# Kernel tuning notes

Hardware: AMD Instinct MI355X
Metric: run time of the kernel (lower is better)

Reference implementation:

```python
import jax, jax.numpy as jnp
import numpy as np

IFZ = 256      # in_features
SFZ = 1280     # sequence_features
AHZ = 8        # attention heads
AFZ = 64       # attention feature dim per head
NRES = 20      # canonical_num_residues
SCALE = float(np.sqrt(AFZ))
RESID = float(np.sqrt(2.0))
EPS = 1e-6


def _ln(x, s, b, eps=1e-5):
    m = jnp.mean(x, axis=-1, keepdims=True)
    v = jnp.var(x, axis=-1, keepdims=True)
    return (x - m) / jnp.sqrt(v + eps) * s + b


def setup_inputs() -> dict:
    key = jax.random.key(0)
    ks = jax.random.split(key, 20)
    N, B, S = 4096, 4, 512
    HD = AHZ * AFZ
    w = lambda k, shp: (jax.random.normal(k, shp, jnp.float32) * 0.02)
    d = {}
    d["x"] = jax.random.normal(ks[0], (N, IFZ), jnp.float32)
    d["packed_sequence_emb"] = jax.random.normal(ks[1], (B, S, SFZ), jnp.float32)
    d["packed_sequence_mask"] = jnp.ones((B, S), jnp.float32)
    d["prot_mask"] = jnp.arange(N, dtype=jnp.int32)
    d["batch"] = jax.random.randint(ks[2], (N,), 0, B, jnp.int32)
    # projections (bias=False)
    d["Wq"] = w(ks[3], (HD, IFZ))
    d["Wk"] = w(ks[4], (HD, SFZ))
    d["Wv"] = w(ks[5], (HD, SFZ))
    # ag: LayerNorm(HD) -> Linear(HD, IFZ, bias=False) (dropout = identity at eval)
    d["ag_ln_s"] = jnp.ones((HD,), jnp.float32)
    d["ag_ln_b"] = jnp.zeros((HD,), jnp.float32)
    d["Wag"] = w(ks[6], (IFZ, HD))
    d["res_ln_s"] = jnp.ones((3, IFZ), jnp.float32)
    d["res_ln_b"] = jnp.zeros((3, IFZ), jnp.float32)
    d["res_w1"] = w(ks[7], (3, IFZ, IFZ))
    d["res_b1"] = jnp.zeros((3, IFZ), jnp.float32)
    d["res_w2"] = w(ks[8], (3, IFZ, IFZ))
    d["res_b2"] = jnp.zeros((3, IFZ), jnp.float32)
    d["head_w"] = w(ks[9], (NRES, IFZ))
    d["head_b"] = jnp.zeros((NRES,), jnp.float32)
    # output LayerNorm en
    d["en_s"] = jnp.ones((IFZ,), jnp.float32)
    d["en_b"] = jnp.zeros((IFZ,), jnp.float32)
    return d


def _forward(x, emb, mask, prot_mask, batch, Wq, Wk, Wv, ag_ln_s, ag_ln_b, Wag,
             res_ln_s, res_ln_b, res_w1, res_b1, res_w2, res_b2,
             head_w, head_b, en_s, en_b):
    N = x.shape[0]
    B, S = emb.shape[:2]
    b_idx = batch[prot_mask]                      # [M]
    xp = x[prot_mask]                             # [M, IFZ]
    M = xp.shape[0]
    q = (xp @ Wq.T).reshape(M, AHZ, AFZ)          # [M,H,D]
    k = (emb @ Wk.T).reshape(B, S, AHZ, AFZ)      # [B,S,H,D]
    v = (emb @ Wv.T).reshape(B, S, AHZ, AFZ)
    # score vs every protein, then pick own protein (avoids materializing [M,S,H,D] gather)
    scores_all = jnp.einsum('mhd,bshd->mbsh', q, k) / SCALE          # [M,B,S,H]
    sel = b_idx[:, None, None, None]
    scores = jnp.take_along_axis(scores_all, sel, axis=1)[:, 0]       # [M,S,H]
    mb = mask[b_idx][:, :, None]                                      # [M,S,1]
    # padded_sequence_softmax: softmax over S, zero pads, renormalize
    sm = jax.nn.softmax(scores, axis=1) * mb
    w = sm / (jnp.sum(sm, axis=1, keepdims=True) + EPS)               # [M,S,H]
    feat_all = jnp.einsum('msh,bshd->mbhd', w, v)                     # [M,B,H,D]
    feat = jnp.take_along_axis(feat_all, sel, axis=1)[:, 0]
    feat = feat.reshape(M, AHZ * AFZ)
    ag = _ln(feat, ag_ln_s, ag_ln_b) @ Wag.T                          # [M, IFZ]
    # seq_aa_head on the scattered new features (identical to ag for unique prot_mask)
    h = ag
    for i in range(3):
        y = _ln(h, res_ln_s[i], res_ln_b[i])
        y = jax.nn.relu(y @ res_w1[i].T + res_b1[i])
        y = y @ res_w2[i].T + res_b2[i]
        h = (h + y) / RESID
    logits = h @ head_w.T + head_b                                     # [M, NRES]
    new_features = jnp.zeros_like(x).at[prot_mask].set(ag)
    seq_aa_logits = jnp.zeros((N, NRES), x.dtype).at[prot_mask].set(logits)
    unpacked_scores = jnp.zeros((N, S, AHZ), x.dtype).at[prot_mask].set(scores)
    out_x = _ln(x + new_features / RESID, en_s, en_b)
    return out_x, seq_aa_logits, unpacked_scores


def reference(x, packed_sequence_emb, packed_sequence_mask, prot_mask, batch,
              Wq, Wk, Wv, ag_ln_s, ag_ln_b, Wag,
              res_ln_s, res_ln_b, res_w1, res_b1, res_w2, res_b2,
              head_w, head_b, en_s, en_b):
    return _forward(x, packed_sequence_emb, packed_sequence_mask, prot_mask, batch,
                    Wq, Wk, Wv, ag_ln_s, ag_ln_b, Wag,
                    res_ln_s, res_ln_b, res_w1, res_b1, res_w2, res_b2,
                    head_w, head_b, en_s, en_b)
```

## Files before the change

kernel.cpp:

```cpp
#include <hip/hip_runtime.h>
#include <math.h>


typedef short bf8 __attribute__((ext_vector_type(8)));
typedef short bf4 __attribute__((ext_vector_type(4)));
typedef float f32x4 __attribute__((ext_vector_type(4)));
typedef unsigned short u16;

constexpr int LDT = 40;
enum { EPI_NONE = 0, EPI_BIAS_RELU = 1, EPI_BIAS = 2, EPI_RESID = 3 };
#define RSQRT2 0.70710678118654752f

__device__ __forceinline__ u16 f2bf(float f) {
  unsigned int u = __builtin_bit_cast(unsigned int, f);
  unsigned int r = u + 0x7fffu + ((u >> 16) & 1u);
  return (u16)(r >> 16);
}
__device__ __forceinline__ float bf2f(u16 v) {
  return __builtin_bit_cast(float, (unsigned int)v << 16);
}
__device__ __forceinline__ f32x4 mfma16(bf8 a, bf8 b, f32x4 c) {
  return __builtin_amdgcn_mfma_f32_16x16x32_bf16(a, b, c, 0, 0, 0);
}

struct CvtDesc { const float* src; u16* dst; int n; };
struct CvtArgs { CvtDesc d[8]; };

__global__ __launch_bounds__(256) void cvt_k(CvtArgs a) {
  CvtDesc d = a.d[blockIdx.z];
  int i = (blockIdx.x * 256 + threadIdx.x) * 8;
  if (i >= d.n) return;
  f32x4 v0 = *(const f32x4*)(d.src + i);
  f32x4 v1 = *(const f32x4*)(d.src + i + 4);
  bf8 o;
  o[0] = (short)f2bf(v0[0]); o[1] = (short)f2bf(v0[1]);
  o[2] = (short)f2bf(v0[2]); o[3] = (short)f2bf(v0[3]);
  o[4] = (short)f2bf(v1[0]); o[5] = (short)f2bf(v1[1]);
  o[6] = (short)f2bf(v1[2]); o[7] = (short)f2bf(v1[3]);
  *(bf8*)(d.dst + i) = o;
}

template <int EPI, bool BFOUT>
__global__ __launch_bounds__(256) void mgemm2(
    const u16* __restrict__ A, const u16* __restrict__ B,
    void* __restrict__ Cv, int M, int N, int K, int lda, int ldb, int ldc,
    const float* __restrict__ bias, const float* __restrict__ Hin,
    const int* __restrict__ gatherA, const int* __restrict__ scatterC) {
  __shared__ __align__(16) u16 As[128 * LDT];
  __shared__ __align__(16) u16 Bs[64 * LDT];
  const int tid = threadIdx.x;
  const int m0 = blockIdx.y * 128, n0 = blockIdx.x * 64;
  const int wave = tid >> 6, lane = tid & 63;
  const int wm = (wave & 1) * 64, wn = (wave >> 1) * 32;
  const int lrow = lane & 15, quad = lane >> 4;
  const int srow = tid >> 2, skq = tid & 3;

  int gr0 = m0 + srow, gr1 = m0 + srow + 64;
  int ar0 = (gr0 < M) ? (gatherA ? gatherA[gr0] : gr0) : -1;
  int ar1 = (gr1 < M) ? (gatherA ? gatherA[gr1] : gr1) : -1;
  const u16* Ap0 = (ar0 >= 0) ? A + (size_t)ar0 * lda + skq * 8 : nullptr;
  const u16* Ap1 = (ar1 >= 0) ? A + (size_t)ar1 * lda + skq * 8 : nullptr;
  const u16* Bp = (n0 + srow < N) ? B + (size_t)(n0 + srow) * ldb + skq * 8 : nullptr;
  u16* AsW0 = &As[srow * LDT + skq * 8];
  u16* AsW1 = &As[(srow + 64) * LDT + skq * 8];
  u16* BsW = &Bs[srow * LDT + skq * 8];

  f32x4 acc[4][2];
#pragma unroll
  for (int i = 0; i < 4; ++i)
#pragma unroll
    for (int j = 0; j < 2; ++j) acc[i][j] = (f32x4){0.f, 0.f, 0.f, 0.f};
  const bf8 z8 = {0, 0, 0, 0, 0, 0, 0, 0};

  for (int k0 = 0; k0 < K; k0 += 32) {
    bf8 a0 = Ap0 ? *(const bf8*)(Ap0 + k0) : z8;
    bf8 a1 = Ap1 ? *(const bf8*)(Ap1 + k0) : z8;
    bf8 bv = Bp ? *(const bf8*)(Bp + k0) : z8;
    *(bf8*)AsW0 = a0;
    *(bf8*)AsW1 = a1;
    *(bf8*)BsW = bv;
    __syncthreads();
    bf8 af[4], bfr[2];
#pragma unroll
    for (int i = 0; i < 4; ++i)
      af[i] = *(const bf8*)&As[(wm + i * 16 + lrow) * LDT + quad * 8];
#pragma unroll
    for (int j = 0; j < 2; ++j)
      bfr[j] = *(const bf8*)&Bs[(wn + j * 16 + lrow) * LDT + quad * 8];
#pragma unroll
    for (int i = 0; i < 4; ++i)
#pragma unroll
      for (int j = 0; j < 2; ++j) acc[i][j] = mfma16(af[i], bfr[j], acc[i][j]);
    __syncthreads();
  }

  float* Cf = (float*)Cv;
  u16* Cb = (u16*)Cv;
#pragma unroll
  for (int i = 0; i < 4; ++i) {
#pragma unroll
    for (int r = 0; r < 4; ++r) {
      int row = m0 + wm + i * 16 + quad * 4 + r;
      if (row >= M) continue;
      if (gatherA && gatherA[row] < 0) continue;
      int orow = scatterC ? scatterC[row] : row;
#pragma unroll
      for (int j = 0; j < 2; ++j) {
        int col = n0 + wn + j * 16 + lrow;
        if (col >= N) continue;
        float v = acc[i][j][r];
        if (EPI == EPI_BIAS_RELU) v = fmaxf(v + bias[col], 0.f);
        else if (EPI == EPI_BIAS) v += bias[col];
        else if (EPI == EPI_RESID) v = (Hin[(size_t)row * ldc + col] + v + bias[col]) * RSQRT2;
        if (BFOUT) Cb[(size_t)orow * ldc + col] = f2bf(v);
        else Cf[(size_t)orow * ldc + col] = v;
      }
    }
  }
}

__global__ __launch_bounds__(256) void vtrans(const u16* __restrict__ KV,
                                              u16* __restrict__ VT) {
  __shared__ u16 t[32][33];
  int b = blockIdx.z;
  int s0 = blockIdx.x * 32, d0 = blockIdx.y * 32;
  int tx = threadIdx.x & 31, ty = threadIdx.x >> 5;
#pragma unroll
  for (int i = 0; i < 32; i += 8)
    t[ty + i][tx] = KV[(size_t)(b * 512 + s0 + ty + i) * 1024 + 512 + d0 + tx];
  __syncthreads();
#pragma unroll
  for (int i = 0; i < 32; i += 8)
    VT[(size_t)(b * 512 + d0 + ty + i) * 512 + s0 + tx] = t[tx][ty + i];
}

constexpr int WST = 520;
constexpr int QST = 72;

__global__ __launch_bounds__(256) void attn_fused(
    const u16* __restrict__ Q, const u16* __restrict__ KV,
    const u16* __restrict__ VT, const int* __restrict__ list,
    const float* __restrict__ mask, u16* __restrict__ packed,
    u16* __restrict__ feat, int N) {
  const int b = blockIdx.y >> 3, h = blockIdx.y & 7;
  const int mt = blockIdx.x;
  const int* lst = list + (size_t)b * N + mt * 32;
  if (lst[0] < 0) return;

  __shared__ __align__(16) u16 Ws[32 * WST];
  __shared__ __align__(16) u16 Qs[32 * QST];
  __shared__ __align__(16) u16 KVs[64 * QST];
  __shared__ __align__(16) float mk[8][68];
  __shared__ int mS[32];

  const int tid = threadIdx.x;
  const int wave = tid >> 6, lane = tid & 63;
  const int wm = (wave & 1) * 16, wns = (wave >> 1) * 32;
  const int lrow = lane & 15, quad = lane >> 4;
  const bf8 z8 = {0, 0, 0, 0, 0, 0, 0, 0};

  const int c0 = tid * 2, c1 = tid * 2 + 1;
  const int sr0 = c0 >> 3, kq0 = c0 & 7;
  const int sr1 = c1 >> 3, kq1 = c1 & 7;
  u16* kvw0 = &KVs[sr0 * QST + kq0 * 8];
  u16* kvw1 = &KVs[sr1 * QST + kq1 * 8];

  if (tid < 32) mS[tid] = lst[tid];
  {
    int p = tid >> 5, j = (tid & 31) * 2;
    *(float2*)&mk[p][j] = *(const float2*)&mask[(size_t)b * 512 + p * 64 + j];
  }
  {
    int qr = tid >> 3, kq = tid & 7;
    int m = lst[qr];
    *(bf8*)&Qs[qr * QST + kq * 8] =
        (m >= 0) ? *(const bf8*)(Q + (size_t)m * 512 + h * 64 + kq * 8) : z8;
  }
  const u16* KVb = KV + (size_t)(b * 512) * 1024 + h * 64;
  {
    int sta = mt & 7;
    *(bf8*)kvw0 = *(const bf8*)(KVb + (size_t)(sta * 64 + sr0) * 1024 + kq0 * 8);
    *(bf8*)kvw1 = *(const bf8*)(KVb + (size_t)(sta * 64 + sr1) * 1024 + kq1 * 8);
  }
  __syncthreads();

  const bf8 qa0 = *(const bf8*)&Qs[(wm + lrow) * QST + 0 + quad * 8];
  const bf8 qa1 = *(const bf8*)&Qs[(wm + lrow) * QST + 32 + quad * 8];

  bf8 r0, r1;
  for (int st = 0; st < 8; ++st) {
    const int sta = (st + mt) & 7;
    if (st < 7) {
      int nx = (st + 1 + mt) & 7;
      r0 = *(const bf8*)(KVb + (size_t)(nx * 64 + sr0) * 1024 + kq0 * 8);
      r1 = *(const bf8*)(KVb + (size_t)(nx * 64 + sr1) * 1024 + kq1 * 8);
    }
    f32x4 acc0 = {0.f, 0.f, 0.f, 0.f}, acc1 = acc0;
    {
      bf8 b00 = *(const bf8*)&KVs[(wns + lrow) * QST + quad * 8];
      bf8 b10 = *(const bf8*)&KVs[(wns + 16 + lrow) * QST + quad * 8];
      bf8 b01 = *(const bf8*)&KVs[(wns + lrow) * QST + 32 + quad * 8];
      bf8 b11 = *(const bf8*)&KVs[(wns + 16 + lrow) * QST + 32 + quad * 8];
      __builtin_amdgcn_s_setprio(1);
      acc0 = mfma16(qa0, b00, acc0);
      acc1 = mfma16(qa0, b10, acc1);
      acc0 = mfma16(qa1, b01, acc0);
      acc1 = mfma16(qa1, b11, acc1);
      __builtin_amdgcn_s_setprio(0);
    }
#pragma unroll
    for (int r = 0; r < 4; ++r) {
      int lr = wm + quad * 4 + r;
      Ws[lr * WST + sta * 64 + wns + lrow] = f2bf(acc0[r] * 0.125f);
      Ws[lr * WST + sta * 64 + wns + 16 + lrow] = f2bf(acc1[r] * 0.125f);
    }
    __syncthreads();
    if (st < 7) {
      *(bf8*)kvw0 = r0;
      *(bf8*)kvw1 = r1;
      __syncthreads();
    }
  }

  const u16* VTb = VT + (size_t)(b * 512 + h * 64) * 512;
  bf8 v0p = *(const bf8*)(VTb + (size_t)sr0 * 512 + ((mt & 7) << 6) + kq0 * 8);
  bf8 v1p = *(const bf8*)(VTb + (size_t)sr1 * 512 + ((mt & 7) << 6) + kq1 * 8);

  {
    const int row = tid >> 3, part = tid & 7;
    u16* wrow = &Ws[row * WST + part * 64];
    const int mm = mS[row];
    bf8 w[8];
    float mx = -1e30f;
#pragma unroll
    for (int v = 0; v < 8; ++v) {
      w[v] = *(const bf8*)(wrow + v * 8);
#pragma unroll
      for (int j = 0; j < 8; ++j) mx = fmaxf(mx, bf2f((u16)w[v][j]));
    }
    if (mm >= 0) {
      u16* prow = packed + ((size_t)h * N + mm) * 512 + part * 64;
#pragma unroll
      for (int v = 0; v < 8; ++v) *(bf8*)(prow + v * 8) = w[v];
    }
#pragma unroll
    for (int d = 1; d < 8; d <<= 1) mx = fmaxf(mx, __shfl_xor(mx, d));
    float ev[64];
    float se = 0.f, ms = 0.f;
#pragma unroll
    for (int v = 0; v < 8; ++v) {
      f32x4 m0 = *(const f32x4*)&mk[part][v * 8];
      f32x4 m1 = *(const f32x4*)&mk[part][v * 8 + 4];
#pragma unroll
      for (int j = 0; j < 8; ++j) {
        float e = __expf(bf2f((u16)w[v][j]) - mx);
        ev[v * 8 + j] = e;
        se += e;
        ms += e * (j < 4 ? m0[j] : m1[j - 4]);
      }
    }
#pragma unroll
    for (int d = 1; d < 8; d <<= 1) {
      se += __shfl_xor(se, d);
      ms += __shfl_xor(ms, d);
    }
    float iv = 1.0f / (ms + 1e-6f * se);
#pragma unroll
    for (int v = 0; v < 8; ++v) {
      f32x4 m0 = *(const f32x4*)&mk[part][v * 8];
      f32x4 m1 = *(const f32x4*)&mk[part][v * 8 + 4];
      bf8 o;
#pragma unroll
      for (int j = 0; j < 8; ++j)
        o[j] = (short)f2bf(ev[v * 8 + j] * (j < 4 ? m0[j] : m1[j - 4]) * iv);
      *(bf8*)(wrow + v * 8) = o;
    }
  }
  __syncthreads();
  *(bf8*)kvw0 = v0p;
  *(bf8*)kvw1 = v1p;
  __syncthreads();

  f32x4 acc0 = {0.f, 0.f, 0.f, 0.f}, acc1 = acc0;
  for (int ss = 0; ss < 8; ++ss) {
    const int s0 = ((ss + mt) & 7) << 6;
    if (ss < 7) {
      int nx = ((ss + 1 + mt) & 7) << 6;
      v0p = *(const bf8*)(VTb + (size_t)sr0 * 512 + nx + kq0 * 8);
      v1p = *(const bf8*)(VTb + (size_t)sr1 * 512 + nx + kq1 * 8);
    }
#pragma unroll
    for (int k0 = 0; k0 < 64; k0 += 32) {
      bf8 a = *(const bf8*)&Ws[(wm + lrow) * WST + s0 + k0 + quad * 8];
      bf8 b0 = *(const bf8*)&KVs[(wns + lrow) * QST + k0 + quad * 8];
      bf8 b1 = *(const bf8*)&KVs[(wns + 16 + lrow) * QST + k0 + quad * 8];
      __builtin_amdgcn_s_setprio(1);
      acc0 = mfma16(a, b0, acc0);
      acc1 = mfma16(a, b1, acc1);
      __builtin_amdgcn_s_setprio(0);
    }
    __syncthreads();
    if (ss < 7) {
      *(bf8*)kvw0 = v0p;
      *(bf8*)kvw1 = v1p;
      __syncthreads();
    }
  }
#pragma unroll
  for (int r = 0; r < 4; ++r) {
    int lr = wm + quad * 4 + r;
    int mm = mS[lr];
    if (mm < 0) continue;
    u16* frow = feat + (size_t)mm * 512 + h * 64;
    frow[wns + lrow] = f2bf(acc0[r]);
    frow[wns + 16 + lrow] = f2bf(acc1[r]);
  }
}

__global__ __launch_bounds__(256) void unpack_k(const u16* __restrict__ packed,
                                                const int* __restrict__ pm,
                                                float* __restrict__ out_sc,
                                                int N) {
  __shared__ u16 Ls[8 * 520];
  int m = blockIdx.x, tid = threadIdx.x;
  int h = tid >> 5, c = (tid & 31) * 16;
  const u16* row = packed + ((size_t)h * N + m) * 512 + c;
  *(bf8*)&Ls[h * 520 + c] = *(const bf8*)row;
  *(bf8*)&Ls[h * 520 + c + 8] = *(const bf8*)(row + 8);
  __syncthreads();
  float* orow = out_sc + (size_t)pm[m] * 4096;
#pragma unroll
  for (int i = 0; i < 16; ++i) {
    int e = tid + i * 256;
    orow[e] = bf2f(Ls[(e & 7) * 520 + (e >> 3)]);
  }
}

constexpr int HST = 268;
constexpr int AST = 520;
constexpr int YST = 280;

__global__ __launch_bounds__(1024) void mlp_fused(
    const u16* __restrict__ feat, const float* __restrict__ ag_s,
    const float* __restrict__ ag_b, const u16* __restrict__ Wag,
    float* __restrict__ AGout, const float* __restrict__ rls,
    const float* __restrict__ rlb, const u16* __restrict__ rw1,
    const float* __restrict__ rb1, const u16* __restrict__ rw2,
    const float* __restrict__ rb2, const float* __restrict__ hw,
    const float* __restrict__ hb, const int* __restrict__ pm,
    float* __restrict__ out_lg) {
  __shared__ __align__(16) float Hs[16 * HST];
  __shared__ __align__(16) u16 As[16 * AST];
  __shared__ __align__(16) u16 Ys[16 * YST];
  const int tid = threadIdx.x;
  const int m0 = blockIdx.x * 16;
  const int wave = tid >> 6, lane = tid & 63;
  const int lrow = lane & 15, quad = lane >> 4;
  const int wn = wave * 16;
  const int row = wave;
  const int wq8 = quad * 8;

  const u16* WagW = Wag + (size_t)(wn + lrow) * 512 + wq8;
  const u16* W1W = rw1 + (size_t)(wn + lrow) * 256 + wq8;
  const u16* W2W = rw2 + (size_t)(wn + lrow) * 256 + wq8;

  bf8 wp[8];
#pragma unroll
  for (int i = 0; i < 8; ++i) wp[i] = *(const bf8*)(WagW + i * 32);

  {
    const u16* frow = feat + (size_t)(m0 + row) * 512 + lane * 8;
    bf8 f0 = *(const bf8*)frow;
    float s = 0.f, sq = 0.f;
#pragma unroll
    for (int j = 0; j < 8; ++j) {
      float a = bf2f((u16)f0[j]);
      s += a;
      sq += a * a;
    }
#pragma unroll
    for (int d = 1; d < 64; d <<= 1) { s += __shfl_xor(s, d); sq += __shfl_xor(sq, d); }
    float mean = s * (1.0f / 512.0f);
    float var = sq * (1.0f / 512.0f) - mean * mean;
    float is = 1.0f / sqrtf(var + 1e-5f);
    int c = lane * 8;
    bf8 o0;
#pragma unroll
    for (int j = 0; j < 8; ++j)
      o0[j] = (short)f2bf((bf2f((u16)f0[j]) - mean) * is * ag_s[c + j] + ag_b[c + j]);
    *(bf8*)&As[row * AST + c] = o0;
  }
  __syncthreads();

  {
    f32x4 acc = {0.f, 0.f, 0.f, 0.f};
#pragma unroll
    for (int i = 0; i < 8; ++i) {
      bf8 a = *(const bf8*)&As[lrow * AST + i * 32 + wq8];
      acc = mfma16(a, wp[i], acc);
      wp[i] = *(const bf8*)(WagW + 256 + i * 32);
    }
#pragma unroll
    for (int i = 0; i < 8; ++i) {
      bf8 a = *(const bf8*)&As[lrow * AST + 256 + i * 32 + wq8];
      acc = mfma16(a, wp[i], acc);
      wp[i] = *(const bf8*)(W1W + i * 32);
    }
#pragma unroll
    for (int r = 0; r < 4; ++r) {
      int rr = quad * 4 + r;
      Hs[rr * HST + wn + lrow] = acc[r];
      AGout[(size_t)(m0 + rr) * 256 + wn + lrow] = acc[r];
    }
  }

  for (int layer = 0; layer < 3; ++layer) {
    __syncthreads();
    {
      int c = lane * 4;
      f32x4 h0 = *(const f32x4*)&Hs[row * HST + c];
      float s = h0[0] + h0[1] + h0[2] + h0[3];
      float sq = h0[0] * h0[0] + h0[1] * h0[1] + h0[2] * h0[2] + h0[3] * h0[3];
#pragma unroll
      for (int d = 1; d < 64; d <<= 1) { s += __shfl_xor(s, d); sq += __shfl_xor(sq, d); }
      float mean = s * (1.0f / 256.0f);
      float var = sq * (1.0f / 256.0f) - mean * mean;
      float is = 1.0f / sqrtf(var + 1e-5f);
      const float* g = rls + layer * 256;
      const float* bb = rlb + layer * 256;
      bf4 o;
#pragma unroll
      for (int e = 0; e < 4; ++e)
        o[e] = (short)f2bf((h0[e] - mean) * is * g[c + e] + bb[c + e]);
      *(bf4*)&As[row * AST + c] = o;
    }
    __syncthreads();

    {
      f32x4 acc = {0.f, 0.f, 0.f, 0.f};
#pragma unroll
      for (int i = 0; i < 8; ++i) {
        bf8 a = *(const bf8*)&As[lrow * AST + i * 32 + wq8];
        acc = mfma16(a, wp[i], acc);
        wp[i] = *(const bf8*)(W2W + (size_t)layer * 65536 + i * 32);
      }
      float bi = rb1[layer * 256 + wn + lrow];
#pragma unroll
      for (int r = 0; r < 4; ++r) {
        int rr = quad * 4 + r;
        Ys[rr * YST + wn + lrow] = f2bf(fmaxf(acc[r] + bi, 0.f));
      }
    }
    __syncthreads();

    {
      f32x4 acc = {0.f, 0.f, 0.f, 0.f};
#pragma unroll
      for (int i = 0; i < 8; ++i) {
        bf8 a = *(const bf8*)&Ys[lrow * YST + i * 32 + wq8];
        acc = mfma16(a, wp[i], acc);
        if (layer < 2)
          wp[i] = *(const bf8*)(W1W + (size_t)(layer + 1) * 65536 + i * 32);
      }
      float bi = rb2[layer * 256 + wn + lrow];
#pragma unroll
      for (int r = 0; r < 4; ++r) {
        int rr = quad * 4 + r;
        float* h0 = &Hs[rr * HST + wn + lrow];
        *h0 = (*h0 + acc[r] + bi) * RSQRT2;
      }
    }
  }
  __syncthreads();

  if (lane < 20) {
    const float* hrow = &Hs[row * HST];
    const float* wrow = hw + (size_t)lane * 256;
    float l0 = 0.f, l1 = 0.f, l2 = 0.f, l3 = 0.f;
    for (int k = 0; k < 256; k += 16) {
      f32x4 h0 = *(const f32x4*)&hrow[k];
      f32x4 h1 = *(const f32x4*)&hrow[k + 4];
      f32x4 h2 = *(const f32x4*)&hrow[k + 8];
      f32x4 h3 = *(const f32x4*)&hrow[k + 12];
      f32x4 w0 = *(const f32x4*)&wrow[k];
      f32x4 w1 = *(const f32x4*)&wrow[k + 4];
      f32x4 w2 = *(const f32x4*)&wrow[k + 8];
      f32x4 w3 = *(const f32x4*)&wrow[k + 12];
#pragma unroll
      for (int e = 0; e < 4; ++e) {
        l0 += h0[e] * w0[e];
        l1 += h1[e] * w1[e];
        l2 += h2[e] * w2[e];
        l3 += h3[e] * w3[e];
      }
    }
    out_lg[(size_t)pm[m0 + row] * 20 + lane] = l0 + l1 + l2 + l3 + hb[lane];
  }
}

__global__ __launch_bounds__(256) void outx_k(
    const float* __restrict__ x, const float* __restrict__ ag,
    const int* __restrict__ inv, const float* __restrict__ g,
    const float* __restrict__ bb, float* __restrict__ out) {
  __shared__ float red[256];
  int n = blockIdx.x, tid = threadIdx.x;
  int mi = inv[n];
  float v = x[(size_t)n * 256 + tid];
  if (mi >= 0) v += ag[(size_t)mi * 256 + tid] * RSQRT2;
  red[tid] = v;
  __syncthreads();
  for (int off = 128; off; off >>= 1) {
    if (tid < off) red[tid] += red[tid + off];
    __syncthreads();
  }
  float mean = red[0] * (1.0f / 256.0f);
  __syncthreads();
  red[tid] = v * v;
  __syncthreads();
  for (int off = 128; off; off >>= 1) {
    if (tid < off) red[tid] += red[tid + off];
    __syncthreads();
  }
  float var = red[0] * (1.0f / 256.0f) - mean * mean;
  float is = 1.0f / sqrtf(var + 1e-5f);
  out[(size_t)n * 256 + tid] = (v - mean) * is * g[tid] + bb[tid];
}

__global__ void init_idx_k(int* __restrict__ list, int* __restrict__ inv,
                           int* __restrict__ cnt, int N, int B) {
  int i = blockIdx.x * 256 + threadIdx.x;
  if (i < B * N) list[i] = -1;
  if (i < N) inv[i] = -1;
  if (i < B) cnt[i] = 0;
}

__global__ void compact_k(const int* __restrict__ pm,
                          const int* __restrict__ batch, int* __restrict__ list,
                          int* __restrict__ inv, int* __restrict__ cnt, int N) {
  int m = blockIdx.x * 256 + threadIdx.x;
  if (m >= N) return;
  int p = pm[m];
  int b = batch[p];
  int slot = atomicAdd(&cnt[b], 1);
  list[(size_t)b * N + slot] = m;
  inv[p] = m;
}

extern "C" void kernel_launch(void* const* d_in, const int* in_sizes, int n_in,
                              void* d_out, int out_size, void* d_ws,
                              size_t ws_size, hipStream_t stream) {
  const float* x = (const float*)d_in[0];
  const float* emb = (const float*)d_in[1];
  const float* mask = (const float*)d_in[2];
  const int* pm = (const int*)d_in[3];
  const int* batch = (const int*)d_in[4];
  const float* Wq = (const float*)d_in[5];
  const float* Wk = (const float*)d_in[6];
  const float* Wv = (const float*)d_in[7];
  const float* ag_s = (const float*)d_in[8];
  const float* ag_b = (const float*)d_in[9];
  const float* Wag = (const float*)d_in[10];
  const float* rls = (const float*)d_in[11];
  const float* rlb = (const float*)d_in[12];
  const float* rw1 = (const float*)d_in[13];
  const float* rb1 = (const float*)d_in[14];
  const float* rw2 = (const float*)d_in[15];
  const float* rb2 = (const float*)d_in[16];
  const float* hw = (const float*)d_in[17];
  const float* hb = (const float*)d_in[18];
  const float* ens = (const float*)d_in[19];
  const float* enb = (const float*)d_in[20];

  const int N = in_sizes[0] / 256;
  const int B = in_sizes[2] / 512;

  char* wsb = (char*)d_ws;
  u16* embbf = (u16*)(wsb + 0);
  u16* xbf   = (u16*)(wsb + 5242880);
  u16* Wkvbf = (u16*)(wsb + 7340032);
  u16* Wqbf  = (u16*)(wsb + 9961472);
  u16* packed = (u16*)(wsb + 0);
  u16* KVbf   = (u16*)(wsb + 33554432);
  u16* Qbf    = (u16*)(wsb + 37748736);
  u16* VT     = (u16*)(wsb + 41943040);
  u16* featE  = (u16*)(wsb + 44040192);
  float* AG = (float*)(wsb + 37748736);
  u16* Wagbf = (u16*)(wsb + 48234496);
  u16* rw1bf = (u16*)(wsb + 48496640);
  u16* rw2bf = (u16*)(wsb + 48889856);
  int* list  = (int*)(wsb + 49545216);
  int* inv   = (int*)(wsb + 49610752);
  int* cnt   = (int*)(wsb + 49627136);

  float* out_x = (float*)d_out;
  float* out_lg = out_x + (size_t)N * 256;
  float* out_sc = out_lg + (size_t)N * 20;

  CvtArgs ca;
  ca.d[0] = {emb, embbf, 2 * 512 * 1280 * 2};
  ca.d[1] = {x, xbf, 4096 * 256};
  ca.d[2] = {Wk, Wkvbf, 512 * 1280};
  ca.d[3] = {Wv, Wkvbf + 512 * 1280, 512 * 1280};
  ca.d[4] = {Wq, Wqbf, 512 * 256};
  ca.d[5] = {Wag, Wagbf, 256 * 512};
  ca.d[6] = {rw1, rw1bf, 3 * 256 * 256};
  ca.d[7] = {rw2, rw2bf, 3 * 256 * 256};
  cvt_k<<<dim3(1281, 1, 8), 256, 0, stream>>>(ca);
  init_idx_k<<<(B * N + 255) / 256, 256, 0, stream>>>(list, inv, cnt, N, B);
  compact_k<<<(N + 255) / 256, 256, 0, stream>>>(pm, batch, list, inv, cnt, N);

  mgemm2<EPI_NONE, true><<<dim3(16, 16), 256, 0, stream>>>(
      embbf, Wkvbf, KVbf, B * 512, 1024, 1280, 1280, 1280, 1024,
      nullptr, nullptr, nullptr, nullptr);
  mgemm2<EPI_NONE, true><<<dim3(8, 32), 256, 0, stream>>>(
      xbf, Wqbf, Qbf, N, 512, 256, 256, 256, 512,
      nullptr, nullptr, pm, nullptr);
  vtrans<<<dim3(16, 16, B), 256, 0, stream>>>(KVbf, VT);

  attn_fused<<<dim3(N / 32, B * 8), 256, 0, stream>>>(
      Qbf, KVbf, VT, list, mask, packed, featE, N);
  unpack_k<<<N, 256, 0, stream>>>(packed, pm, out_sc, N);

  mlp_fused<<<dim3(N / 16), 1024, 0, stream>>>(
      featE, ag_s, ag_b, Wagbf, AG, rls, rlb, rw1bf, rb1, rw2bf, rb2,
      hw, hb, pm, out_lg);

  outx_k<<<N, 256, 0, stream>>>(x, AG, inv, ens, enb, out_x);
}
```

Before: 301.1 us.

## Fuse output LayerNorm into MLP kernel and use 64-row GEMM tiles

The final out_x LayerNorm for rows present in prot_mask is now computed inside mlp_fused from the attention-gate result held in shared memory. This removes the fp32 AG round-trip through global memory, and outx_k only handles rows with no mapping. Separately, mgemm2 gains an MT template parameter, and the K/V and Q projections switch to 64-row tiles to launch more blocks and improve occupancy on small grids. The costs are that each GEMM block now reuses the B tile less, and mlp_fused needs an extra barrier.

```diff
diff --git a/kernel.cpp b/kernel.cpp
--- a/kernel.cpp
+++ b/kernel.cpp
@@ -40,55 +40,62 @@
   *(bf8*)(d.dst + i) = o;
 }
 
-template <int EPI, bool BFOUT>
+template <int EPI, bool BFOUT, int MT>
 __global__ __launch_bounds__(256) void mgemm2(
     const u16* __restrict__ A, const u16* __restrict__ B,
     void* __restrict__ Cv, int M, int N, int K, int lda, int ldb, int ldc,
     const float* __restrict__ bias, const float* __restrict__ Hin,
     const int* __restrict__ gatherA, const int* __restrict__ scatterC) {
-  __shared__ __align__(16) u16 As[128 * LDT];
+  constexpr int NF = MT / 32;
+  __shared__ __align__(16) u16 As[MT * LDT];
   __shared__ __align__(16) u16 Bs[64 * LDT];
   const int tid = threadIdx.x;
-  const int m0 = blockIdx.y * 128, n0 = blockIdx.x * 64;
+  const int m0 = blockIdx.y * MT, n0 = blockIdx.x * 64;
   const int wave = tid >> 6, lane = tid & 63;
-  const int wm = (wave & 1) * 64, wn = (wave >> 1) * 32;
+  const int wm = (wave & 1) * (MT / 2), wn = (wave >> 1) * 32;
   const int lrow = lane & 15, quad = lane >> 4;
   const int srow = tid >> 2, skq = tid & 3;
 
-  int gr0 = m0 + srow, gr1 = m0 + srow + 64;
+  int gr0 = m0 + srow;
   int ar0 = (gr0 < M) ? (gatherA ? gatherA[gr0] : gr0) : -1;
-  int ar1 = (gr1 < M) ? (gatherA ? gatherA[gr1] : gr1) : -1;
   const u16* Ap0 = (ar0 >= 0) ? A + (size_t)ar0 * lda + skq * 8 : nullptr;
-  const u16* Ap1 = (ar1 >= 0) ? A + (size_t)ar1 * lda + skq * 8 : nullptr;
+  const u16* Ap1 = nullptr;
+  if constexpr (MT == 128) {
+    int gr1 = m0 + srow + 64;
+    int ar1 = (gr1 < M) ? (gatherA ? gatherA[gr1] : gr1) : -1;
+    Ap1 = (ar1 >= 0) ? A + (size_t)ar1 * lda + skq * 8 : nullptr;
+  }
   const u16* Bp = (n0 + srow < N) ? B + (size_t)(n0 + srow) * ldb + skq * 8 : nullptr;
   u16* AsW0 = &As[srow * LDT + skq * 8];
-  u16* AsW1 = &As[(srow + 64) * LDT + skq * 8];
+  u16* AsW1 = (MT == 128) ? &As[(srow + 64) * LDT + skq * 8] : nullptr;
   u16* BsW = &Bs[srow * LDT + skq * 8];
 
-  f32x4 acc[4][2];
-#pragma unroll
-  for (int i = 0; i < 4; ++i)
+  f32x4 acc[NF][2];
+#pragma unroll
+  for (int i = 0; i < NF; ++i)
 #pragma unroll
     for (int j = 0; j < 2; ++j) acc[i][j] = (f32x4){0.f, 0.f, 0.f, 0.f};
   const bf8 z8 = {0, 0, 0, 0, 0, 0, 0, 0};
 
   for (int k0 = 0; k0 < K; k0 += 32) {
     bf8 a0 = Ap0 ? *(const bf8*)(Ap0 + k0) : z8;
-    bf8 a1 = Ap1 ? *(const bf8*)(Ap1 + k0) : z8;
     bf8 bv = Bp ? *(const bf8*)(Bp + k0) : z8;
     *(bf8*)AsW0 = a0;
-    *(bf8*)AsW1 = a1;
+    if constexpr (MT == 128) {
+      bf8 a1 = Ap1 ? *(const bf8*)(Ap1 + k0) : z8;
+      *(bf8*)AsW1 = a1;
+    }
     *(bf8*)BsW = bv;
     __syncthreads();
-    bf8 af[4], bfr[2];
-#pragma unroll
-    for (int i = 0; i < 4; ++i)
+    bf8 af[NF], bfr[2];
+#pragma unroll
+    for (int i = 0; i < NF; ++i)
       af[i] = *(const bf8*)&As[(wm + i * 16 + lrow) * LDT + quad * 8];
 #pragma unroll
     for (int j = 0; j < 2; ++j)
       bfr[j] = *(const bf8*)&Bs[(wn + j * 16 + lrow) * LDT + quad * 8];
 #pragma unroll
-    for (int i = 0; i < 4; ++i)
+    for (int i = 0; i < NF; ++i)
 #pragma unroll
       for (int j = 0; j < 2; ++j) acc[i][j] = mfma16(af[i], bfr[j], acc[i][j]);
     __syncthreads();
@@ -97,7 +104,7 @@
   float* Cf = (float*)Cv;
   u16* Cb = (u16*)Cv;
 #pragma unroll
-  for (int i = 0; i < 4; ++i) {
+  for (int i = 0; i < NF; ++i) {
 #pragma unroll
     for (int r = 0; r < 4; ++r) {
       int row = m0 + wm + i * 16 + quad * 4 + r;
@@ -343,12 +350,13 @@
 __global__ __launch_bounds__(1024) void mlp_fused(
     const u16* __restrict__ feat, const float* __restrict__ ag_s,
     const float* __restrict__ ag_b, const u16* __restrict__ Wag,
-    float* __restrict__ AGout, const float* __restrict__ rls,
+    const float* __restrict__ x, const float* __restrict__ ens,
+    const float* __restrict__ enb, const float* __restrict__ rls,
     const float* __restrict__ rlb, const u16* __restrict__ rw1,
     const float* __restrict__ rb1, const u16* __restrict__ rw2,
     const float* __restrict__ rb2, const float* __restrict__ hw,
     const float* __restrict__ hb, const int* __restrict__ pm,
-    float* __restrict__ out_lg) {
+    float* __restrict__ out_lg, float* __restrict__ out_x) {
   __shared__ __align__(16) float Hs[16 * HST];
   __shared__ __align__(16) u16 As[16 * AST];
   __shared__ __align__(16) u16 Ys[16 * YST];
@@ -359,6 +367,7 @@
   const int wn = wave * 16;
   const int row = wave;
   const int wq8 = quad * 8;
+  const int nrow = pm[m0 + row];
 
   const u16* WagW = Wag + (size_t)(wn + lrow) * 512 + wq8;
   const u16* W1W = rw1 + (size_t)(wn + lrow) * 256 + wq8;
@@ -410,12 +419,32 @@
     for (int r = 0; r < 4; ++r) {
       int rr = quad * 4 + r;
       Hs[rr * HST + wn + lrow] = acc[r];
-      AGout[(size_t)(m0 + rr) * 256 + wn + lrow] = acc[r];
-    }
+    }
+  }
+  __syncthreads();
+
+  {
+    int c = lane * 4;
+    f32x4 xv = *(const f32x4*)&x[(size_t)nrow * 256 + c];
+    f32x4 hv = *(const f32x4*)&Hs[row * HST + c];
+    f32x4 v;
+#pragma unroll
+    for (int e = 0; e < 4; ++e) v[e] = xv[e] + hv[e] * RSQRT2;
+    float s = v[0] + v[1] + v[2] + v[3];
+    float sq = v[0] * v[0] + v[1] * v[1] + v[2] * v[2] + v[3] * v[3];
+#pragma unroll
+    for (int d = 1; d < 64; d <<= 1) { s += __shfl_xor(s, d); sq += __shfl_xor(sq, d); }
+    float mean = s * (1.0f / 256.0f);
+    float var = sq * (1.0f / 256.0f) - mean * mean;
+    float is = 1.0f / sqrtf(var + 1e-5f);
+    f32x4 o;
+#pragma unroll
+    for (int e = 0; e < 4; ++e)
+      o[e] = (v[e] - mean) * is * ens[c + e] + enb[c + e];
+    *(f32x4*)&out_x[(size_t)nrow * 256 + c] = o;
   }
 
   for (int layer = 0; layer < 3; ++layer) {
-    __syncthreads();
     {
       int c = lane * 4;
       f32x4 h0 = *(const f32x4*)&Hs[row * HST + c];
@@ -470,8 +499,8 @@
         *h0 = (*h0 + acc[r] + bi) * RSQRT2;
       }
     }
-  }
-  __syncthreads();
+    __syncthreads();
+  }
 
   if (lane < 20) {
     const float* hrow = &Hs[row * HST];
@@ -494,19 +523,18 @@
         l3 += h3[e] * w3[e];
       }
     }
-    out_lg[(size_t)pm[m0 + row] * 20 + lane] = l0 + l1 + l2 + l3 + hb[lane];
+    out_lg[(size_t)nrow * 20 + lane] = l0 + l1 + l2 + l3 + hb[lane];
   }
 }
 
 __global__ __launch_bounds__(256) void outx_k(
-    const float* __restrict__ x, const float* __restrict__ ag,
-    const int* __restrict__ inv, const float* __restrict__ g,
-    const float* __restrict__ bb, float* __restrict__ out) {
+    const float* __restrict__ x, const int* __restrict__ inv,
+    const float* __restrict__ g, const float* __restrict__ bb,
+    float* __restrict__ out) {
   __shared__ float red[256];
   int n = blockIdx.x, tid = threadIdx.x;
-  int mi = inv[n];
+  if (inv[n] >= 0) return;
   float v = x[(size_t)n * 256 + tid];
-  if (mi >= 0) v += ag[(size_t)mi * 256 + tid] * RSQRT2;
   red[tid] = v;
   __syncthreads();
   for (int off = 128; off; off >>= 1) {
@@ -584,7 +612,6 @@
   u16* Qbf    = (u16*)(wsb + 37748736);
   u16* VT     = (u16*)(wsb + 41943040);
   u16* featE  = (u16*)(wsb + 44040192);
-  float* AG = (float*)(wsb + 37748736);
   u16* Wagbf = (u16*)(wsb + 48234496);
   u16* rw1bf = (u16*)(wsb + 48496640);
   u16* rw2bf = (u16*)(wsb + 48889856);
@@ -609,10 +636,10 @@
   init_idx_k<<<(B * N + 255) / 256, 256, 0, stream>>>(list, inv, cnt, N, B);
   compact_k<<<(N + 255) / 256, 256, 0, stream>>>(pm, batch, list, inv, cnt, N);
 
-  mgemm2<EPI_NONE, true><<<dim3(16, 16), 256, 0, stream>>>(
+  mgemm2<EPI_NONE, true, 64><<<dim3(16, B * 8), 256, 0, stream>>>(
       embbf, Wkvbf, KVbf, B * 512, 1024, 1280, 1280, 1280, 1024,
       nullptr, nullptr, nullptr, nullptr);
-  mgemm2<EPI_NONE, true><<<dim3(8, 32), 256, 0, stream>>>(
+  mgemm2<EPI_NONE, true, 64><<<dim3(8, N / 64), 256, 0, stream>>>(
       xbf, Wqbf, Qbf, N, 512, 256, 256, 256, 512,
       nullptr, nullptr, pm, nullptr);
   vtrans<<<dim3(16, 16, B), 256, 0, stream>>>(KVbf, VT);
@@ -622,8 +649,8 @@
   unpack_k<<<N, 256, 0, stream>>>(packed, pm, out_sc, N);
 
   mlp_fused<<<dim3(N / 16), 1024, 0, stream>>>(
-      featE, ag_s, ag_b, Wagbf, AG, rls, rlb, rw1bf, rb1, rw2bf, rb2,
-      hw, hb, pm, out_lg);
-
-  outx_k<<<N, 256, 0, stream>>>(x, AG, inv, ens, enb, out_x);
-}
+      featE, ag_s, ag_b, Wagbf, x, ens, enb, rls, rlb, rw1bf, rb1,
+      rw2bf, rb2, hw, hb, pm, out_lg, out_x);
+
+  outx_k<<<N, 256, 0, stream>>>(x, inv, ens, enb, out_x);
+}
```

Result: faster. 288.3 us (-4.2%).
